# Kernel optimization log

Hardware: AMD Instinct MI355X
Metric: run time of the kernel (lower is better)

## Reference

```python
import jax, jax.numpy as jnp
import numpy as np
import math

B, S, D, H, HD, BS = 8, 1024, 1024, 16, 64, 8  # batch, seq, dim, heads, head_dim, blk_size
ROPE_BASE = 10000.0


def setup_inputs() -> dict:
    key = jax.random.key(0)
    ks = jax.random.split(key, 5)
    std = 1.0 / math.sqrt(D)
    x = jax.random.normal(ks[0], (B, S, D), dtype=jnp.float32)
    wq = jax.random.normal(ks[1], (D, D), dtype=jnp.float32) * std
    wk = jax.random.normal(ks[2], (D, D), dtype=jnp.float32) * std
    wv = jax.random.normal(ks[3], (D, D), dtype=jnp.float32) * std
    wo = jax.random.normal(ks[4], (D, D), dtype=jnp.float32) * std
    inv_freq = 1.0 / (ROPE_BASE ** (np.arange(0, HD, 2, dtype=np.float32) / HD))
    ang = np.outer(np.arange(S, dtype=np.float32), inv_freq)  # (S, HD/2)
    freqs_cos = jnp.asarray(np.cos(ang), dtype=jnp.float32)
    freqs_sin = jnp.asarray(np.sin(ang), dtype=jnp.float32)
    return {"x": x, "wq": wq, "wk": wk, "wv": wv, "wo": wo,
            "freqs_cos": freqs_cos, "freqs_sin": freqs_sin}


def _rope(t, cos, sin):
    # t: (B, S, H, HD); cos/sin: (S, HD/2); complex-pair rotary (interleaved)
    tr, ti = t[..., 0::2], t[..., 1::2]
    c = cos[None, :, None, :]
    s = sin[None, :, None, :]
    out_r = tr * c - ti * s
    out_i = tr * s + ti * c
    return jnp.stack([out_r, out_i], axis=-1).reshape(t.shape)


def reference(x, wq, wk, wv, wo, freqs_cos, freqs_sin):
    b, s, _ = x.shape
    q = (x @ wq).reshape(b, s, H, HD)
    k = (x @ wk).reshape(b, s, H, HD)
    v = (x @ wv).reshape(b, s, H, HD)
    q = _rope(q, freqs_cos, freqs_sin)
    k = _rope(k, freqs_cos, freqs_sin)
    # block-causal mask: query attends to any key whose block index <= its own
    pos = jnp.arange(s)
    allowed = (pos[None, :] // BS) <= (pos[:, None] // BS)  # (S, S)
    scale = 1.0 / math.sqrt(HD)
    scores = jnp.einsum("bqhd,bkhd->bhqk", q, k) * scale
    scores = jnp.where(allowed[None, None], scores, jnp.finfo(scores.dtype).min)
    probs = jax.nn.softmax(scores, axis=-1)
    out = jnp.einsum("bhqk,bkhd->bqhd", probs, v).reshape(b, s, H * HD)
    return out @ wo
```

## Files before the change

kernel.cpp:

```cpp
#include <hip/hip_runtime.h>
#include <stdint.h>

#define BATCH 8
#define SEQ 1024
#define DMODEL 1024
#define NHEAD 16
#define HDIM 64
#define MROWS (BATCH * SEQ)
#define NQKV (3 * DMODEL)
#define SCALE_LOG2E 0.18033688011112043f

typedef __bf16 bf16x8 __attribute__((ext_vector_type(8)));
typedef float f32x4 __attribute__((ext_vector_type(4)));
typedef unsigned short u16x8 __attribute__((ext_vector_type(8)));
typedef unsigned short u16x4 __attribute__((ext_vector_type(4)));

static __device__ __forceinline__ unsigned short f2bf(float f) {
  unsigned int u = __builtin_bit_cast(unsigned int, f);
  u += 0x7fffu + ((u >> 16) & 1u);
  return (unsigned short)(u >> 16);
}
static __device__ __forceinline__ float bf2f(unsigned short h) {
  unsigned int u = ((unsigned int)h) << 16;
  return __builtin_bit_cast(float, u);
}
static __device__ __forceinline__ void async_cp16(void* lds, const void* g) {
  __builtin_amdgcn_global_load_lds((const __attribute__((address_space(1))) void*)g,
                                   (__attribute__((address_space(3))) void*)lds, 16, 0, 0);
}

__global__ void k_cvt_x(const float* __restrict__ x, unsigned short* __restrict__ xb) {
  const size_t i = ((size_t)blockIdx.x * 256 + threadIdx.x) * 4;
  const float4 v = *(const float4*)(x + i);
  u16x4 o;
  o[0] = f2bf(v.x); o[1] = f2bf(v.y); o[2] = f2bf(v.z); o[3] = f2bf(v.w);
  *(u16x4*)(xb + i) = o;
}

__global__ void k_cvt_w(const float* __restrict__ wq, const float* __restrict__ wk,
                        const float* __restrict__ wv, const float* __restrict__ wo,
                        unsigned short* __restrict__ wqkvT, unsigned short* __restrict__ woT) {
  __shared__ float tile[64][65];
  const int z = blockIdx.z;
  const float* w = (z == 0) ? wq : (z == 1) ? wk : (z == 2) ? wv : wo;
  unsigned short* dst = (z < 3) ? (wqkvT + (size_t)z * DMODEL * DMODEL) : woT;
  const int n0 = blockIdx.x * 64, k0 = blockIdx.y * 64;
  for (int i = threadIdx.x; i < 4096; i += 256) {
    const int r = i >> 6, c = i & 63;
    tile[r][c] = w[(size_t)(k0 + r) * DMODEL + n0 + c];
  }
  __syncthreads();
  for (int i = threadIdx.x; i < 4096; i += 256) {
    const int r = i >> 6, c = i & 63;
    dst[(size_t)(n0 + r) * DMODEL + k0 + c] = f2bf(tile[c][r]);
  }
}

template <int NOUT, bool F32OUT>
__global__ __launch_bounds__(256) void k_gemm(const unsigned short* __restrict__ A,
                                              const unsigned short* __restrict__ Bt,
                                              void* __restrict__ Cout) {
  constexpr int K = DMODEL;
  constexpr int GX = NOUT / 128;
  __shared__ unsigned short Al[128 * 32];
  __shared__ unsigned short Bl[128 * 32];
  const int nwg = gridDim.x;
  const int o = blockIdx.x;
  const int t = (o & 7) * (nwg >> 3) + (o >> 3);
  const int tm = (t / GX) * 128, tn = (t % GX) * 128;
  const int tid = threadIdx.x;
  const int lane = tid & 63, wid = tid >> 6;
  const int wm = wid >> 1, wn = wid & 1;
  const int fr = lane & 15, fq = lane >> 4;

  f32x4 acc[4][4];
#pragma unroll
  for (int i = 0; i < 4; ++i)
#pragma unroll
    for (int j = 0; j < 4; ++j) acc[i][j] = (f32x4){0.f, 0.f, 0.f, 0.f};

  const int o0 = wid * 2048 + lane * 16;
  const int row0 = o0 >> 6;
  const int ce0 = (o0 & 63) >> 1;

  for (int kk = 0; kk < K; kk += 32) {
    async_cp16((char*)Al + wid * 2048,        A + (size_t)(tm + row0) * K + kk + ce0);
    async_cp16((char*)Al + wid * 2048 + 1024, A + (size_t)(tm + row0 + 16) * K + kk + ce0);
    async_cp16((char*)Bl + wid * 2048,        Bt + (size_t)(tn + row0) * K + kk + ce0);
    async_cp16((char*)Bl + wid * 2048 + 1024, Bt + (size_t)(tn + row0 + 16) * K + kk + ce0);
    __syncthreads();
    bf16x8 af[4], bf[4];
#pragma unroll
    for (int mi = 0; mi < 4; ++mi)
      af[mi] = *(const bf16x8*)(Al + (wm * 64 + mi * 16 + fr) * 32 + fq * 8);
#pragma unroll
    for (int ni = 0; ni < 4; ++ni)
      bf[ni] = *(const bf16x8*)(Bl + (wn * 64 + ni * 16 + fr) * 32 + fq * 8);
#pragma unroll
    for (int mi = 0; mi < 4; ++mi)
#pragma unroll
      for (int ni = 0; ni < 4; ++ni)
        acc[mi][ni] = __builtin_amdgcn_mfma_f32_16x16x32_bf16(af[mi], bf[ni], acc[mi][ni], 0, 0, 0);
    __syncthreads();
  }

#pragma unroll
  for (int mi = 0; mi < 4; ++mi) {
    const int row = tm + wm * 64 + mi * 16 + fq * 4;
#pragma unroll
    for (int ni = 0; ni < 4; ++ni) {
      const int col = tn + wn * 64 + ni * 16 + fr;
      if constexpr (F32OUT) {
        float* C = (float*)Cout;
#pragma unroll
        for (int r = 0; r < 4; ++r) C[(size_t)(row + r) * NOUT + col] = acc[mi][ni][r];
      } else {
        unsigned short* C = (unsigned short*)Cout;
#pragma unroll
        for (int r = 0; r < 4; ++r) C[(size_t)(row + r) * NOUT + col] = f2bf(acc[mi][ni][r]);
      }
    }
  }
}

__global__ void k_rope(const unsigned short* __restrict__ qkv, const float* __restrict__ fc,
                       const float* __restrict__ fs, unsigned short* __restrict__ qr,
                       unsigned short* __restrict__ kr) {
  const int idx = blockIdx.x * 256 + threadIdx.x;
  const int row = idx >> 9;
  const int rem = idx & 511;
  const int h = rem >> 5, pr = rem & 31;
  const int s = row & (SEQ - 1), b = row >> 10;
  const size_t src = (size_t)row * NQKV + h * HDIM + 2 * pr;
  const size_t dst = ((size_t)(b * NHEAD + h) * SEQ + s) * HDIM + 2 * pr;
  const float c = fc[s * 32 + pr], sn = fs[s * 32 + pr];
  float tr = bf2f(qkv[src]), ti = bf2f(qkv[src + 1]);
  qr[dst] = f2bf(tr * c - ti * sn);
  qr[dst + 1] = f2bf(tr * sn + ti * c);
  tr = bf2f(qkv[src + DMODEL]); ti = bf2f(qkv[src + DMODEL + 1]);
  kr[dst] = f2bf(tr * c - ti * sn);
  kr[dst + 1] = f2bf(tr * sn + ti * c);
}

__global__ __launch_bounds__(256) void k_tv(const unsigned short* __restrict__ qkv,
                                            unsigned short* __restrict__ vt) {
  __shared__ unsigned short t[64][72];
  const int sb = blockIdx.x, bh = blockIdx.y;
  const int b = bh >> 4, h = bh & 15;
  const int tid = threadIdx.x;
  const int r0 = tid >> 3, c8 = (tid & 7) * 8;
#pragma unroll
  for (int p = 0; p < 2; ++p) {
    const int s = p * 32 + r0;
    *(u16x8*)&t[s][c8] =
        *(const u16x8*)(qkv + (size_t)(b * SEQ + sb * 64 + s) * NQKV + 2 * DMODEL + h * HDIM + c8);
  }
  __syncthreads();
#pragma unroll
  for (int p = 0; p < 2; ++p) {
    const int d = p * 32 + r0;
    u16x8 v;
#pragma unroll
    for (int j = 0; j < 8; ++j) v[j] = t[c8 + j][d];
    *(u16x8*)(vt + ((size_t)(bh * HDIM + d)) * SEQ + sb * 64 + c8) = v;
  }
}

__global__ __launch_bounds__(256) void k_attn(const unsigned short* __restrict__ qr,
                                              const unsigned short* __restrict__ kr,
                                              const unsigned short* __restrict__ vt,
                                              unsigned short* __restrict__ ao) {
  const int o = blockIdx.x, nwg = gridDim.x;
  const int t = (o & 7) * (nwg >> 3) + (o >> 3);
  const int qt = 15 - (t & 15);
  const int bh = t >> 4;
  const int tid = threadIdx.x, lane = tid & 63, w = tid >> 6;
  const int fr = lane & 15, fq = lane >> 4;
  __shared__ unsigned short Ks[2][4096];
  __shared__ unsigned short Vs[2][4096];
  __shared__ unsigned short Ps[4][1024];
  const size_t base = (size_t)bh * SEQ * HDIM;
  const char* kgb = (const char*)(kr + base);
  const char* vgb = (const char*)(vt + base);

  const int qrow = qt * 64 + w * 16 + fr;
  const bf16x8 qf0 = *(const bf16x8*)(qr + base + (size_t)qrow * HDIM + fq * 8);
  const bf16x8 qf1 = *(const bf16x8*)(qr + base + (size_t)qrow * HDIM + 32 + fq * 8);
  const int qblk = (w * 16 + fr) >> 3;
  const int swz = (fr & 7) << 4;

  f32x4 oacc[4];
#pragma unroll
  for (int i = 0; i < 4; ++i) oacc[i] = (f32x4){0.f, 0.f, 0.f, 0.f};
  float m = -3.0e38f, l = 0.f;

  auto stage = [&](int kt, int bb) {
#pragma unroll
    for (int c = 0; c < 2; ++c) {
      const int dstb = c * 4096 + tid * 16;
      const int row = dstb >> 7;
      const int col = (dstb & 127) ^ ((row & 7) << 4);
      char* kl = (char*)Ks[bb] + c * 4096 + (tid >> 6) * 1024;
      char* vl = (char*)Vs[bb] + c * 4096 + (tid >> 6) * 1024;
      async_cp16(kl, kgb + (size_t)kt * 8192 + row * 128 + col);
      async_cp16(vl, vgb + (size_t)row * 2048 + kt * 128 + col);
    }
  };

  stage(0, 0);
  int buf = 0;
  for (int kt = 0; kt <= qt; ++kt) {
    const bool pre = (kt < qt);
    if (pre) {
      stage(kt + 1, buf ^ 1);
      asm volatile("s_waitcnt vmcnt(4)" ::: "memory");
    } else {
      asm volatile("s_waitcnt vmcnt(0)" ::: "memory");
    }
    __builtin_amdgcn_s_barrier();
    __builtin_amdgcn_sched_barrier(0);
    const char* Kb = (const char*)Ks[buf];
    const char* Vb = (const char*)Vs[buf];

    f32x4 sc[4];
#pragma unroll
    for (int kb = 0; kb < 4; ++kb) {
      const int rowb = (16 * kb + fr) * 128;
      const bf16x8 k0 = *(const bf16x8*)(Kb + rowb + ((16 * fq) ^ swz));
      const bf16x8 k1 = *(const bf16x8*)(Kb + rowb + ((64 + 16 * fq) ^ swz));
      sc[kb] = __builtin_amdgcn_mfma_f32_16x16x32_bf16(k0, qf0, (f32x4){0.f, 0.f, 0.f, 0.f}, 0, 0, 0);
      sc[kb] = __builtin_amdgcn_mfma_f32_16x16x32_bf16(k1, qf1, sc[kb], 0, 0, 0);
    }
    if (kt == qt) {
#pragma unroll
      for (int kb = 0; kb < 4; ++kb)
        if (2 * kb + (fq >> 1) > qblk) sc[kb] = (f32x4){-3.0e38f, -3.0e38f, -3.0e38f, -3.0e38f};
    }
    float pmax = sc[0][0];
#pragma unroll
    for (int kb = 0; kb < 4; ++kb)
#pragma unroll
      for (int r = 0; r < 4; ++r) pmax = fmaxf(pmax, sc[kb][r]);
    pmax = fmaxf(pmax, __shfl_xor(pmax, 16));
    pmax = fmaxf(pmax, __shfl_xor(pmax, 32));
    const float mnew = fmaxf(m, pmax);
    const float corr = __builtin_amdgcn_exp2f((m - mnew) * SCALE_LOG2E);
    m = mnew;
    float rs = 0.f;
#pragma unroll
    for (int kb = 0; kb < 4; ++kb)
#pragma unroll
      for (int r = 0; r < 4; ++r) {
        const float p = __builtin_amdgcn_exp2f((sc[kb][r] - mnew) * SCALE_LOG2E);
        sc[kb][r] = p;
        rs += p;
      }
    rs += __shfl_xor(rs, 16);
    rs += __shfl_xor(rs, 32);
    l = l * corr + rs;
#pragma unroll
    for (int db = 0; db < 4; ++db) oacc[db] *= corr;
#pragma unroll
    for (int kb = 0; kb < 4; ++kb) {
      u16x4 pv;
#pragma unroll
      for (int r = 0; r < 4; ++r) pv[r] = f2bf(sc[kb][r]);
      *(u16x4*)((char*)Ps[w] + fr * 128 + ((32 * kb + 8 * fq) ^ swz)) = pv;
    }
    asm volatile("s_waitcnt lgkmcnt(0)" ::: "memory");
    __builtin_amdgcn_sched_barrier(0);
    const bf16x8 pf0 = *(const bf16x8*)((const char*)Ps[w] + fr * 128 + ((16 * fq) ^ swz));
    const bf16x8 pf1 = *(const bf16x8*)((const char*)Ps[w] + fr * 128 + ((64 + 16 * fq) ^ swz));
#pragma unroll
    for (int db = 0; db < 4; ++db) {
      const int rowb = (16 * db + fr) * 128;
      const bf16x8 v0 = *(const bf16x8*)(Vb + rowb + ((16 * fq) ^ swz));
      const bf16x8 v1 = *(const bf16x8*)(Vb + rowb + ((64 + 16 * fq) ^ swz));
      oacc[db] = __builtin_amdgcn_mfma_f32_16x16x32_bf16(v0, pf0, oacc[db], 0, 0, 0);
      oacc[db] = __builtin_amdgcn_mfma_f32_16x16x32_bf16(v1, pf1, oacc[db], 0, 0, 0);
    }
    asm volatile("s_waitcnt lgkmcnt(0)" ::: "memory");
    __builtin_amdgcn_sched_barrier(0);
    __builtin_amdgcn_s_barrier();
    buf ^= 1;
  }
  const float inv = 1.f / l;
  const int b = bh >> 4, h = bh & 15;
  const int qg = qt * 64 + w * 16 + fr;
#pragma unroll
  for (int db = 0; db < 4; ++db) {
    u16x4 ov;
#pragma unroll
    for (int r = 0; r < 4; ++r) ov[r] = f2bf(oacc[db][r] * inv);
    *(u16x4*)(ao + (size_t)(b * SEQ + qg) * DMODEL + h * HDIM + 16 * db + 4 * fq) = ov;
  }
}

extern "C" void kernel_launch(void* const* d_in, const int* in_sizes, int n_in,
                              void* d_out, int out_size, void* d_ws, size_t ws_size,
                              hipStream_t stream) {
  (void)in_sizes; (void)n_in; (void)out_size; (void)ws_size;
  const float* x = (const float*)d_in[0];
  const float* wq = (const float*)d_in[1];
  const float* wk = (const float*)d_in[2];
  const float* wv = (const float*)d_in[3];
  const float* wo = (const float*)d_in[4];
  const float* fc = (const float*)d_in[5];
  const float* fs = (const float*)d_in[6];
  float* out = (float*)d_out;

  unsigned short* xb = (unsigned short*)d_ws;
  unsigned short* wqkvT = xb + (size_t)MROWS * DMODEL;
  unsigned short* woT = wqkvT + (size_t)NQKV * DMODEL;
  unsigned short* qrb = woT + (size_t)DMODEL * DMODEL;
  unsigned short* krb = qrb + (size_t)MROWS * DMODEL;
  unsigned short* vtb = krb + (size_t)MROWS * DMODEL;
  unsigned short* qkvr = vtb + (size_t)MROWS * DMODEL;
  unsigned short* aob = qkvr;

  k_cvt_x<<<MROWS * DMODEL / 1024, 256, 0, stream>>>(x, xb);
  k_cvt_w<<<dim3(16, 16, 4), 256, 0, stream>>>(wq, wk, wv, wo, wqkvT, woT);
  k_gemm<NQKV, false><<<(NQKV / 128) * (MROWS / 128), 256, 0, stream>>>(xb, wqkvT, qkvr);
  k_rope<<<MROWS * 512 / 256, 256, 0, stream>>>(qkvr, fc, fs, qrb, krb);
  k_tv<<<dim3(16, BATCH * NHEAD), 256, 0, stream>>>(qkvr, vtb);
  k_attn<<<16 * BATCH * NHEAD, 256, 0, stream>>>(qrb, krb, vtb, aob);
  k_gemm<DMODEL, true><<<(DMODEL / 128) * (MROWS / 128), 256, 0, stream>>>(aob, woT, out);
}
```

Measured before the change: 274.9 us.

## Fuse RoPE and V transpose into QKV GEMM epilogue

```diff
diff --git a/kernel.cpp b/kernel.cpp
--- a/kernel.cpp
+++ b/kernel.cpp
@@ -123,46 +123,94 @@
   }
 }
 
-__global__ void k_rope(const unsigned short* __restrict__ qkv, const float* __restrict__ fc,
-                       const float* __restrict__ fs, unsigned short* __restrict__ qr,
-                       unsigned short* __restrict__ kr) {
-  const int idx = blockIdx.x * 256 + threadIdx.x;
-  const int row = idx >> 9;
-  const int rem = idx & 511;
-  const int h = rem >> 5, pr = rem & 31;
-  const int s = row & (SEQ - 1), b = row >> 10;
-  const size_t src = (size_t)row * NQKV + h * HDIM + 2 * pr;
-  const size_t dst = ((size_t)(b * NHEAD + h) * SEQ + s) * HDIM + 2 * pr;
-  const float c = fc[s * 32 + pr], sn = fs[s * 32 + pr];
-  float tr = bf2f(qkv[src]), ti = bf2f(qkv[src + 1]);
-  qr[dst] = f2bf(tr * c - ti * sn);
-  qr[dst + 1] = f2bf(tr * sn + ti * c);
-  tr = bf2f(qkv[src + DMODEL]); ti = bf2f(qkv[src + DMODEL + 1]);
-  kr[dst] = f2bf(tr * c - ti * sn);
-  kr[dst + 1] = f2bf(tr * sn + ti * c);
-}
-
-__global__ __launch_bounds__(256) void k_tv(const unsigned short* __restrict__ qkv,
-                                            unsigned short* __restrict__ vt) {
-  __shared__ unsigned short t[64][72];
-  const int sb = blockIdx.x, bh = blockIdx.y;
-  const int b = bh >> 4, h = bh & 15;
+__global__ __launch_bounds__(256) void k_gemm_qkv(const unsigned short* __restrict__ A,
+                                                  const unsigned short* __restrict__ Bt,
+                                                  const float* __restrict__ fc,
+                                                  const float* __restrict__ fs,
+                                                  unsigned short* __restrict__ qr,
+                                                  unsigned short* __restrict__ kr,
+                                                  unsigned short* __restrict__ vt) {
+  constexpr int K = DMODEL;
+  constexpr int GX = NQKV / 128;
+  __shared__ unsigned short Al[128 * 32];
+  __shared__ unsigned short Bl[128 * 32];
+  const int nwg = gridDim.x;
+  const int o = blockIdx.x;
+  const int t = (o & 7) * (nwg >> 3) + (o >> 3);
+  const int tm = (t / GX) * 128, tn = (t % GX) * 128;
   const int tid = threadIdx.x;
-  const int r0 = tid >> 3, c8 = (tid & 7) * 8;
-#pragma unroll
-  for (int p = 0; p < 2; ++p) {
-    const int s = p * 32 + r0;
-    *(u16x8*)&t[s][c8] =
-        *(const u16x8*)(qkv + (size_t)(b * SEQ + sb * 64 + s) * NQKV + 2 * DMODEL + h * HDIM + c8);
-  }
-  __syncthreads();
-#pragma unroll
-  for (int p = 0; p < 2; ++p) {
-    const int d = p * 32 + r0;
-    u16x8 v;
-#pragma unroll
-    for (int j = 0; j < 8; ++j) v[j] = t[c8 + j][d];
-    *(u16x8*)(vt + ((size_t)(bh * HDIM + d)) * SEQ + sb * 64 + c8) = v;
+  const int lane = tid & 63, wid = tid >> 6;
+  const int wm = wid >> 1, wn = wid & 1;
+  const int fr = lane & 15, fq = lane >> 4;
+
+  f32x4 acc[4][4];
+#pragma unroll
+  for (int i = 0; i < 4; ++i)
+#pragma unroll
+    for (int j = 0; j < 4; ++j) acc[i][j] = (f32x4){0.f, 0.f, 0.f, 0.f};
+
+  const int o0 = wid * 2048 + lane * 16;
+  const int row0 = o0 >> 6;
+  const int ce0 = (o0 & 63) >> 1;
+
+  for (int kk = 0; kk < K; kk += 32) {
+    async_cp16((char*)Al + wid * 2048,        A + (size_t)(tm + row0) * K + kk + ce0);
+    async_cp16((char*)Al + wid * 2048 + 1024, A + (size_t)(tm + row0 + 16) * K + kk + ce0);
+    async_cp16((char*)Bl + wid * 2048,        Bt + (size_t)(tn + row0) * K + kk + ce0);
+    async_cp16((char*)Bl + wid * 2048 + 1024, Bt + (size_t)(tn + row0 + 16) * K + kk + ce0);
+    __syncthreads();
+    bf16x8 af[4], bf[4];
+#pragma unroll
+    for (int mi = 0; mi < 4; ++mi)
+      af[mi] = *(const bf16x8*)(Al + (wm * 64 + mi * 16 + fr) * 32 + fq * 8);
+#pragma unroll
+    for (int ni = 0; ni < 4; ++ni)
+      bf[ni] = *(const bf16x8*)(Bl + (wn * 64 + ni * 16 + fr) * 32 + fq * 8);
+#pragma unroll
+    for (int mi = 0; mi < 4; ++mi)
+#pragma unroll
+      for (int ni = 0; ni < 4; ++ni)
+        acc[mi][ni] = __builtin_amdgcn_mfma_f32_16x16x32_bf16(af[mi], bf[ni], acc[mi][ni], 0, 0, 0);
+    __syncthreads();
+  }
+
+  const int typ = tn >> 10;
+  const int hh = ((tn & 1023) >> 6) + wn;
+  if (typ == 2) {
+#pragma unroll
+    for (int mi = 0; mi < 4; ++mi) {
+      const int rowb = tm + wm * 64 + mi * 16 + fq * 4;
+      const int b = rowb >> 10, s0 = rowb & 1023;
+#pragma unroll
+      for (int ni = 0; ni < 4; ++ni) {
+        const int hd = ni * 16 + fr;
+        u16x4 ov;
+#pragma unroll
+        for (int r = 0; r < 4; ++r) ov[r] = f2bf(acc[mi][ni][r]);
+        *(u16x4*)(vt + ((size_t)((b * 16 + hh) * 64 + hd)) * SEQ + s0) = ov;
+      }
+    }
+  } else {
+    unsigned short* dst = (typ == 0) ? qr : kr;
+    const float sgn = (fr & 1) ? 1.0f : -1.0f;
+#pragma unroll
+    for (int mi = 0; mi < 4; ++mi) {
+      const int rowb = tm + wm * 64 + mi * 16 + fq * 4;
+      const int b = rowb >> 10, s0 = rowb & 1023;
+#pragma unroll
+      for (int ni = 0; ni < 4; ++ni) {
+        const int hd = ni * 16 + fr;
+        const int pr = ni * 8 + (fr >> 1);
+#pragma unroll
+        for (int r = 0; r < 4; ++r) {
+          const float a = acc[mi][ni][r];
+          const float p = __shfl_xor(a, 1);
+          const float c = fc[(s0 + r) * 32 + pr];
+          const float sn = fs[(s0 + r) * 32 + pr];
+          dst[((size_t)((b * 16 + hh) * SEQ) + s0 + r) * HDIM + hd] = f2bf(a * c + sgn * (p * sn));
+        }
+      }
+    }
   }
 }
 
@@ -315,14 +363,11 @@
   unsigned short* qrb = woT + (size_t)DMODEL * DMODEL;
   unsigned short* krb = qrb + (size_t)MROWS * DMODEL;
   unsigned short* vtb = krb + (size_t)MROWS * DMODEL;
-  unsigned short* qkvr = vtb + (size_t)MROWS * DMODEL;
-  unsigned short* aob = qkvr;
+  unsigned short* aob = xb;
 
   k_cvt_x<<<MROWS * DMODEL / 1024, 256, 0, stream>>>(x, xb);
   k_cvt_w<<<dim3(16, 16, 4), 256, 0, stream>>>(wq, wk, wv, wo, wqkvT, woT);
-  k_gemm<NQKV, false><<<(NQKV / 128) * (MROWS / 128), 256, 0, stream>>>(xb, wqkvT, qkvr);
-  k_rope<<<MROWS * 512 / 256, 256, 0, stream>>>(qkvr, fc, fs, qrb, krb);
-  k_tv<<<dim3(16, BATCH * NHEAD), 256, 0, stream>>>(qkvr, vtb);
+  k_gemm_qkv<<<(NQKV / 128) * (MROWS / 128), 256, 0, stream>>>(xb, wqkvT, fc, fs, qrb, krb, vtb);
   k_attn<<<16 * BATCH * NHEAD, 256, 0, stream>>>(qrb, krb, vtb, aob);
   k_gemm<DMODEL, true><<<(DMODEL / 128) * (MROWS / 128), 256, 0, stream>>>(aob, woT, out);
 }
```

New measurement: 265.4 us. 1.04x faster.
